# Kernel optimization log

Hardware: AMD Instinct MI355X
Metric: run time of the kernel (lower is better)

Reference implementation:

```python
import jax, jax.numpy as jnp
import numpy as np

EMBED_DIM = 512
Q_DIM = 64
V_DIM = 64
WINDOW_SIZE = 128
B, N = 2, 4096


def setup_inputs() -> dict:
    key = jax.random.key(0)
    ks = jax.random.split(key, 7)
    s = 1.0 / np.sqrt(EMBED_DIM)
    u = lambda k, shape: jax.random.uniform(k, shape, jnp.float32, -s, s)
    return {
        "x": jax.random.normal(ks[0], (B, N, EMBED_DIM), jnp.float32),
        "Wq": u(ks[1], (EMBED_DIM, Q_DIM)),
        "bq": u(ks[2], (Q_DIM,)),
        "Wk": u(ks[3], (EMBED_DIM, Q_DIM)),
        "bk": u(ks[4], (Q_DIM,)),
        "Wv": u(ks[5], (EMBED_DIM, V_DIM)),
        "bv": u(ks[6], (V_DIM,)),
    }


def reference(x, Wq, bq, Wk, bk, Wv, bv):
    b, n, _ = x.shape
    w = WINDOW_SIZE // 2
    Q = x @ Wq + bq  # (b, n, Qd)
    K = x @ Wk + bk  # (b, n, Qd)
    V = x @ Wv + bv  # (b, n, Vd)

    diags = jnp.arange(-w, w + 1)            # (nd,) offsets di
    nd = diags.shape[0]
    # Gather K[i + di] via padded K; invalid positions masked to 0 afterwards.
    Kpad = jnp.pad(K, ((0, 0), (w, w), (0, 0)))
    j = jnp.arange(n)[:, None] + diags[None, :]          # (n, nd) = i + di
    Kg = Kpad[:, j + w, :]                               # (b, n, nd, Qd)
    scores = jnp.einsum('bnd,bnod->bno', Q, Kg)          # (b, n, nd)
    valid = (j >= 0) & (j < n)
    scores = jnp.where(valid[None], scores, 0.0)

    # Faithful to original: diagonal dot products are scattered into the FIRST
    # nd columns of a dense (b, n, n) matrix (rest zeros), softmax over the
    # full n columns, then dense matmul with V.
    columns = jnp.zeros((b, n, n), dtype=x.dtype).at[:, :, :nd].set(scores)
    attn = jax.nn.softmax(columns, axis=2)               # (b, n, n)
    return attn @ V                                      # (b, n, Vd)
```

## Files before the change

kernel.cpp:

```cpp
#include <hip/hip_runtime.h>

typedef _Float16 half8 __attribute__((ext_vector_type(8)));
typedef float f32x4 __attribute__((ext_vector_type(4)));

#define NN 4096
#define NE 512
#define HD 64
#define KROWS 4288
#define KOFF  64
#define WSCALE (1.0f / 256.0f)

__device__ __forceinline__ void f16_split(float f, _Float16& hi, _Float16& lo) {
    hi = (_Float16)f;
    lo = (_Float16)(f - (float)hi);
}

#define MFMA16(a, b, c) __builtin_amdgcn_mfma_f32_16x16x32_f16((a), (b), (c), 0, 0, 0)

__global__ __launch_bounds__(64) void wprep_kernel(
    const float* __restrict__ Wq, const float* __restrict__ Wk,
    const float* __restrict__ Wv,
    _Float16* __restrict__ Wf, _Float16* __restrict__ Khi,
    _Float16* __restrict__ Vf, float* __restrict__ Vs)
{
    const int gtid = blockIdx.x * 64 + threadIdx.x;
    const int L = gtid & 63;
    {
        const int nt = (gtid >> 6) % 12;
        const int kt = gtid / 768;
        const int n = nt * 16 + (L & 15);
        const int kbase = kt * 32 + (L >> 4) * 8;
        const float* src; int col;
        if (n < 64)       { src = Wq; col = n; }
        else if (n < 128) { src = Wk; col = n - 64; }
        else              { src = Wv; col = n - 128; }
        half8 sh;
#pragma unroll
        for (int j = 0; j < 8; ++j)
            sh[j] = (_Float16)src[(size_t)(kbase + j) * HD + col];
        *(half8*)(Wf + (size_t)gtid * 8) = sh;
    }
    if (gtid < 6144) {
        const int p = gtid >> 3, o = gtid & 7;
        const int b = p / 192, q = p - b * 192;
        const size_t row = (size_t)b * KROWS + (q < 64 ? q : 4096 + q);
        const half8 z = {0, 0, 0, 0, 0, 0, 0, 0};
        *(half8*)(Khi + row * HD + o * 8) = z;
    }
    if (gtid < 3200) {
        const int rem = gtid % 1600;
        const int jt = rem / 320;
        const int nt = (rem / 64) % 5;
        half8 sh = {0, 0, 0, 0, 0, 0, 0, 0};
        if (nt == 4 && (L & 15) == 0) {
#pragma unroll
            for (int jj = 0; jj < 8; ++jj) {
                const int j = jt * 32 + (L >> 4) * 8 + jj;
                if (j < 129) sh[jj] = (_Float16)1.0f;
            }
        }
        *(half8*)(Vf + (size_t)gtid * 8) = sh;
    }
    if (gtid < 128) Vs[gtid] = 0.f;
}

__global__ __launch_bounds__(1024, 4) void proj_kernel(
    const float* __restrict__ x, const _Float16* __restrict__ Wf,
    const float* __restrict__ bq, const float* __restrict__ bk,
    const float* __restrict__ bv,
    _Float16* __restrict__ Qhi, _Float16* __restrict__ Qlo,
    _Float16* __restrict__ Khi, _Float16* __restrict__ Vf,
    float* __restrict__ Vs)
{
    __shared__ float parts[2][4][3][64][4];
    __shared__ float V_lds[32][68];
    const int tid = threadIdx.x;
    const int L = tid & 63;
    const int w = tid >> 6;
    const int m = L & 15, kg = L >> 4;
    const int blk = blockIdx.x;
    const int b = blk >> 7;
    const int mt = w >> 3;
    const int t3 = (w >> 1) & 3;
    const int h = w & 1;
    const int r0 = blk * 32;
    const int rr = r0 + mt * 16;

    const float* xp = x + (size_t)(rr + m) * NE + h * 256 + kg * 8;
    const _Float16* wfb = Wf + ((size_t)(h * 8) * 12 + t3 * 3) * 512 + L * 8;

    f32x4 acc[3];
#pragma unroll
    for (int t = 0; t < 3; ++t) acc[t] = (f32x4){0.f, 0.f, 0.f, 0.f};

#pragma unroll
    for (int kt = 0; kt < 8; ++kt) {
        const float4 x0 = *(const float4*)(xp + kt * 32);
        const float4 x1 = *(const float4*)(xp + kt * 32 + 4);
        const float xv[8] = {x0.x, x0.y, x0.z, x0.w, x1.x, x1.y, x1.z, x1.w};
        half8 ahi, alo;
#pragma unroll
        for (int j = 0; j < 8; ++j) {
            _Float16 hh, ll; f16_split(xv[j], hh, ll);
            ahi[j] = hh; alo[j] = ll;
        }
#pragma unroll
        for (int t = 0; t < 3; ++t) {
            const half8 wv = *(const half8*)(wfb + (size_t)kt * 6144 + t * 512);
            acc[t] = MFMA16(ahi, wv, acc[t]);
            acc[t] = MFMA16(alo, wv, acc[t]);
        }
    }

    if (h == 1) {
#pragma unroll
        for (int t = 0; t < 3; ++t)
            *(f32x4*)(&parts[mt][t3][t][L][0]) = acc[t];
    }
    __syncthreads();

    if (h == 0) {
#pragma unroll
        for (int t = 0; t < 3; ++t) {
            const f32x4 p = *(const f32x4*)(&parts[mt][t3][t][L][0]);
            acc[t] += p;
            const int nt = t3 * 3 + t;
            const int cgc = nt * 16 + m;
            const float bias = (cgc < 64) ? bq[cgc]
                             : (cgc < 128) ? bk[cgc - 64] : bv[cgc - 128];
#pragma unroll
            for (int r = 0; r < 4; ++r) {
                const int gr = rr + kg * 4 + r;
                const float val = acc[t][r] + bias;
                if (cgc < 64) {
                    _Float16 hh, ll; f16_split(val, hh, ll);
                    Qhi[(size_t)gr * HD + cgc] = hh;
                    Qlo[(size_t)gr * HD + cgc] = ll;
                } else if (cgc < 128) {
                    const int d = cgc - 64, n = gr & 4095;
                    Khi[((size_t)b * KROWS + KOFF + n) * HD + d] = (_Float16)val;
                } else {
                    V_lds[mt * 16 + kg * 4 + r][cgc - 128] = val;
                }
            }
        }
    }
    __syncthreads();

    if (tid < 64) {
        float s = 0.f;
#pragma unroll
        for (int r = 0; r < 32; ++r) s += V_lds[r][tid];
        atomicAdd(&Vs[b * HD + tid], s);
    }

    {
        const int local = blk & 127;
        if (local < 4 && w < 4) {
            const int jt = local;
            const int nt = w;
            half8 sh;
#pragma unroll
            for (int jj = 0; jj < 8; ++jj)
                sh[jj] = (_Float16)V_lds[kg * 8 + jj][nt * 16 + m];
            const size_t fo = ((size_t)((b * 25 + jt * 5 + nt) * 64 + L)) * 8;
            *(half8*)(Vf + fo) = sh;
        } else if (local == 4 && w < 4 && kg == 0) {
            const int nt = w;
            half8 sh = {0, 0, 0, 0, 0, 0, 0, 0};
            sh[0] = (_Float16)V_lds[0][nt * 16 + m];
            const size_t fo = ((size_t)((b * 25 + 4 * 5 + nt) * 64 + L)) * 8;
            *(half8*)(Vf + fo) = sh;
        }
    }
}

__global__ __launch_bounds__(512) void attn_kernel(
    const _Float16* __restrict__ Qhi, const _Float16* __restrict__ Qlo,
    const _Float16* __restrict__ Khi, const _Float16* __restrict__ Vf,
    const float* __restrict__ Vs, float* __restrict__ out)
{
    __shared__ __align__(16) _Float16 wt_hi[32 * 168];
    __shared__ __align__(16) _Float16 wt_lo[32 * 168];
    __shared__ float den_lds[32];

    const int tid = threadIdx.x;
    const int L = tid & 63;
    const int w = tid >> 6;
    const int m = L & 15, kg = L >> 4;
    const int b = blockIdx.x >> 7;
    const int n0 = (blockIdx.x & 127) * 32;
    const int qt = w & 1;
    const int mt = w >> 2;
    const int nt = w & 3;
    const bool den_wave = (w == 0) || (w == 6);

    const float vs = Vs[b * HD + nt * 16 + m];

    const _Float16* qp  = Qhi + ((size_t)(b * NN + n0 + qt * 16 + m)) * HD + kg * 8;
    const _Float16* qp2 = Qlo + ((size_t)(b * NN + n0 + qt * 16 + m)) * HD + kg * 8;
    const half8 qhi0 = *(const half8*)(qp);
    const half8 qhi1 = *(const half8*)(qp + 32);
    const half8 qlo0 = *(const half8*)(qp2);
    const half8 qlo1 = *(const half8*)(qp2 + 32);

    const int i4 = w >> 1;
    const int f = (i4 == 0) ? 1 : (i4 == 1) ? 2 : (i4 == 2) ? 0 : 3;
    int kts[3]; int nkt;
    kts[0] = f + qt; kts[1] = f + qt + 4; kts[2] = f + qt + 8;
    nkt = (i4 == 2) ? 3 : 2;

    const _Float16* KB = Khi + (size_t)b * KROWS * HD;
    half8 kh0[3], kh1[3];
#pragma unroll
    for (int i = 0; i < 3; ++i) {
        if (i < nkt) {
            const _Float16* kp = KB + (size_t)(n0 + kts[i] * 16 + m) * HD + kg * 8;
            kh0[i] = *(const half8*)(kp);
            kh1[i] = *(const half8*)(kp + 32);
        }
    }

    half8 vhi[5], vh4[5];
#pragma unroll
    for (int jt = 0; jt < 5; ++jt) {
        const size_t fo = ((size_t)((b * 25 + jt * 5 + nt) * 64 + L)) * 8;
        vhi[jt] = *(const half8*)(Vf + fo);
    }
    if (den_wave) {
#pragma unroll
        for (int jt = 0; jt < 5; ++jt) {
            const size_t fo4 = ((size_t)((b * 25 + jt * 5 + 4) * 64 + L)) * 8;
            vh4[jt] = *(const half8*)(Vf + fo4);
        }
    }

    for (int t = tid; t < 2048; t += 512) {
        const int bufsel = t >= 1024;
        const int idx = t & 1023;
        const int q = idx >> 5;
        const int j = 129 + (idx & 31);
        (bufsel ? wt_lo : wt_hi)[q * 168 + j] = (_Float16)0.f;
    }

#pragma unroll
    for (int i = 0; i < 3; ++i) {
        if (i < nkt) {
            f32x4 acc = (f32x4){0.f, 0.f, 0.f, 0.f};
            acc = MFMA16(qhi0, kh0[i], acc);
            acc = MFMA16(qhi1, kh1[i], acc);
            acc = MFMA16(qlo0, kh0[i], acc);
            acc = MFMA16(qlo1, kh1[i], acc);
            const int l = kts[i] * 16 + m;
#pragma unroll
            for (int r = 0; r < 4; ++r) {
                const int q = qt * 16 + kg * 4 + r;
                const int j = l - q;
                if (j >= 0 && j < 129) {
                    const float wval = (__expf(acc[r]) - 1.0f) * WSCALE;
                    _Float16 hh, ll; f16_split(wval, hh, ll);
                    wt_hi[q * 168 + j] = hh;
                    wt_lo[q * 168 + j] = ll;
                }
            }
        }
    }
    __syncthreads();

    f32x4 oacc = (f32x4){0.f, 0.f, 0.f, 0.f};
    f32x4 dacc = (f32x4){0.f, 0.f, 0.f, 0.f};
#pragma unroll
    for (int jt = 0; jt < 5; ++jt) {
        const half8 whi = *(const half8*)(wt_hi + (mt * 16 + m) * 168 + jt * 32 + kg * 8);
        const half8 wlo = *(const half8*)(wt_lo + (mt * 16 + m) * 168 + jt * 32 + kg * 8);
        oacc = MFMA16(whi, vhi[jt], oacc);
        oacc = MFMA16(wlo, vhi[jt], oacc);
        if (den_wave) {
            dacc = MFMA16(whi, vh4[jt], dacc);
            dacc = MFMA16(wlo, vh4[jt], dacc);
        }
    }
    if (den_wave && m == 0) {
#pragma unroll
        for (int r = 0; r < 4; ++r) den_lds[mt * 16 + kg * 4 + r] = dacc[r];
    }
    __syncthreads();

    {
#pragma unroll
        for (int r = 0; r < 4; ++r) {
            const int q = mt * 16 + kg * 4 + r;
            const float val = (vs + 256.0f * oacc[r])
                            / (4096.f + 256.0f * den_lds[q]);
            out[((size_t)(b * NN + n0 + q)) * HD + nt * 16 + m] = val;
        }
    }
}

extern "C" void kernel_launch(void* const* d_in, const int* in_sizes, int n_in,
                              void* d_out, int out_size, void* d_ws, size_t ws_size,
                              hipStream_t stream)
{
    const float* x  = (const float*)d_in[0];
    const float* Wq = (const float*)d_in[1];
    const float* bq = (const float*)d_in[2];
    const float* Wk = (const float*)d_in[3];
    const float* bk = (const float*)d_in[4];
    const float* Wv = (const float*)d_in[5];
    const float* bv = (const float*)d_in[6];
    float* out = (float*)d_out;

    char* ws = (char*)d_ws;
    float*     Vs  = (float*)(ws + 0);
    _Float16*  Khi = (_Float16*)(ws + 512);
    _Float16*  Qhi = (_Float16*)(ws + 1098240);
    _Float16*  Qlo = (_Float16*)(ws + 2146816);
    _Float16*  Wf  = (_Float16*)(ws + 3195392);
    _Float16*  Vf  = (_Float16*)(ws + 3392000);

    wprep_kernel<<<192, 64, 0, stream>>>(Wq, Wk, Wv, Wf, Khi, Vf, Vs);
    proj_kernel<<<256, 1024, 0, stream>>>(x, Wf, bq, bk, bv,
                                          Qhi, Qlo, Khi, Vf, Vs);
    attn_kernel<<<256, 512, 0, stream>>>(Qhi, Qlo, Khi, Vf, Vs, out);
}
```

Measured before the change: 94.76 us.

## Reuse projection weights across two row tiles and drop denominator LDS barrier

The projection kernel now has each wave handle both 16-row tiles over a quarter of the embedding dimension. Each loaded weight fragment therefore feeds twice as many MFMAs, and the partial sums are reduced across four K-splits through a larger LDS buffer. In the attention kernel every wave computes the softmax denominator itself and broadcasts it with a wavefront shuffle, which removes the den_lds array and a __syncthreads. The cost is redundant denominator MFMAs and extra vh4 loads in all waves, plus more accumulator registers and LDS in the projection kernel.

```diff
diff --git a/kernel.cpp b/kernel.cpp
--- a/kernel.cpp
+++ b/kernel.cpp
@@ -72,7 +72,7 @@
     _Float16* __restrict__ Khi, _Float16* __restrict__ Vf,
     float* __restrict__ Vs)
 {
-    __shared__ float parts[2][4][3][64][4];
+    __shared__ float parts[3][4][2][3][64][4];
     __shared__ float V_lds[32][68];
     const int tid = threadIdx.x;
     const int L = tid & 63;
@@ -80,58 +80,70 @@
     const int m = L & 15, kg = L >> 4;
     const int blk = blockIdx.x;
     const int b = blk >> 7;
-    const int mt = w >> 3;
-    const int t3 = (w >> 1) & 3;
-    const int h = w & 1;
+    const int t3 = w & 3;
+    const int h4 = w >> 2;
     const int r0 = blk * 32;
-    const int rr = r0 + mt * 16;
-
-    const float* xp = x + (size_t)(rr + m) * NE + h * 256 + kg * 8;
-    const _Float16* wfb = Wf + ((size_t)(h * 8) * 12 + t3 * 3) * 512 + L * 8;
-
-    f32x4 acc[3];
-#pragma unroll
-    for (int t = 0; t < 3; ++t) acc[t] = (f32x4){0.f, 0.f, 0.f, 0.f};
-
-#pragma unroll
-    for (int kt = 0; kt < 8; ++kt) {
-        const float4 x0 = *(const float4*)(xp + kt * 32);
-        const float4 x1 = *(const float4*)(xp + kt * 32 + 4);
-        const float xv[8] = {x0.x, x0.y, x0.z, x0.w, x1.x, x1.y, x1.z, x1.w};
-        half8 ahi, alo;
+
+    const float* xp = x + (size_t)(r0 + m) * NE + h4 * 128 + kg * 8;
+    const _Float16* wfb = Wf + ((size_t)(h4 * 4) * 12 + t3 * 3) * 512 + L * 8;
+
+    f32x4 acc[2][3];
+#pragma unroll
+    for (int rt = 0; rt < 2; ++rt)
+#pragma unroll
+        for (int t = 0; t < 3; ++t) acc[rt][t] = (f32x4){0.f, 0.f, 0.f, 0.f};
+
+#pragma unroll
+    for (int kt = 0; kt < 4; ++kt) {
+        const float4 a0 = *(const float4*)(xp + kt * 32);
+        const float4 a1 = *(const float4*)(xp + kt * 32 + 4);
+        const float4 c0 = *(const float4*)(xp + 16 * NE + kt * 32);
+        const float4 c1 = *(const float4*)(xp + 16 * NE + kt * 32 + 4);
+        const float av[8] = {a0.x, a0.y, a0.z, a0.w, a1.x, a1.y, a1.z, a1.w};
+        const float cv[8] = {c0.x, c0.y, c0.z, c0.w, c1.x, c1.y, c1.z, c1.w};
+        half8 ahi, alo, chi, clo;
 #pragma unroll
         for (int j = 0; j < 8; ++j) {
-            _Float16 hh, ll; f16_split(xv[j], hh, ll);
-            ahi[j] = hh; alo[j] = ll;
+            _Float16 hh, ll;
+            f16_split(av[j], hh, ll); ahi[j] = hh; alo[j] = ll;
+            f16_split(cv[j], hh, ll); chi[j] = hh; clo[j] = ll;
         }
 #pragma unroll
         for (int t = 0; t < 3; ++t) {
             const half8 wv = *(const half8*)(wfb + (size_t)kt * 6144 + t * 512);
-            acc[t] = MFMA16(ahi, wv, acc[t]);
-            acc[t] = MFMA16(alo, wv, acc[t]);
-        }
-    }
-
-    if (h == 1) {
-#pragma unroll
-        for (int t = 0; t < 3; ++t)
-            *(f32x4*)(&parts[mt][t3][t][L][0]) = acc[t];
+            acc[0][t] = MFMA16(ahi, wv, acc[0][t]);
+            acc[0][t] = MFMA16(alo, wv, acc[0][t]);
+            acc[1][t] = MFMA16(chi, wv, acc[1][t]);
+            acc[1][t] = MFMA16(clo, wv, acc[1][t]);
+        }
+    }
+
+    if (h4 != 0) {
+#pragma unroll
+        for (int rt = 0; rt < 2; ++rt)
+#pragma unroll
+            for (int t = 0; t < 3; ++t)
+                *(f32x4*)(&parts[h4 - 1][t3][rt][t][L][0]) = acc[rt][t];
     }
     __syncthreads();
 
-    if (h == 0) {
+    if (h4 == 0) {
+#pragma unroll
+        for (int rt = 0; rt < 2; ++rt)
 #pragma unroll
         for (int t = 0; t < 3; ++t) {
-            const f32x4 p = *(const f32x4*)(&parts[mt][t3][t][L][0]);
-            acc[t] += p;
+            f32x4 s = acc[rt][t];
+#pragma unroll
+            for (int p = 0; p < 3; ++p)
+                s += *(const f32x4*)(&parts[p][t3][rt][t][L][0]);
             const int nt = t3 * 3 + t;
             const int cgc = nt * 16 + m;
             const float bias = (cgc < 64) ? bq[cgc]
                              : (cgc < 128) ? bk[cgc - 64] : bv[cgc - 128];
 #pragma unroll
             for (int r = 0; r < 4; ++r) {
-                const int gr = rr + kg * 4 + r;
-                const float val = acc[t][r] + bias;
+                const int gr = r0 + rt * 16 + kg * 4 + r;
+                const float val = s[r] + bias;
                 if (cgc < 64) {
                     _Float16 hh, ll; f16_split(val, hh, ll);
                     Qhi[(size_t)gr * HD + cgc] = hh;
@@ -140,7 +152,7 @@
                     const int d = cgc - 64, n = gr & 4095;
                     Khi[((size_t)b * KROWS + KOFF + n) * HD + d] = (_Float16)val;
                 } else {
-                    V_lds[mt * 16 + kg * 4 + r][cgc - 128] = val;
+                    V_lds[rt * 16 + kg * 4 + r][cgc - 128] = val;
                 }
             }
         }
@@ -182,7 +194,6 @@
 {
     __shared__ __align__(16) _Float16 wt_hi[32 * 168];
     __shared__ __align__(16) _Float16 wt_lo[32 * 168];
-    __shared__ float den_lds[32];
 
     const int tid = threadIdx.x;
     const int L = tid & 63;
@@ -193,7 +204,6 @@
     const int qt = w & 1;
     const int mt = w >> 2;
     const int nt = w & 3;
-    const bool den_wave = (w == 0) || (w == 6);
 
     const float vs = Vs[b * HD + nt * 16 + m];
 
@@ -226,13 +236,8 @@
     for (int jt = 0; jt < 5; ++jt) {
         const size_t fo = ((size_t)((b * 25 + jt * 5 + nt) * 64 + L)) * 8;
         vhi[jt] = *(const half8*)(Vf + fo);
-    }
-    if (den_wave) {
-#pragma unroll
-        for (int jt = 0; jt < 5; ++jt) {
-            const size_t fo4 = ((size_t)((b * 25 + jt * 5 + 4) * 64 + L)) * 8;
-            vh4[jt] = *(const half8*)(Vf + fo4);
-        }
+        const size_t fo4 = ((size_t)((b * 25 + jt * 5 + 4) * 64 + L)) * 8;
+        vh4[jt] = *(const half8*)(Vf + fo4);
     }
 
     for (int t = tid; t < 2048; t += 512) {
@@ -275,23 +280,21 @@
         const half8 wlo = *(const half8*)(wt_lo + (mt * 16 + m) * 168 + jt * 32 + kg * 8);
         oacc = MFMA16(whi, vhi[jt], oacc);
         oacc = MFMA16(wlo, vhi[jt], oacc);
-        if (den_wave) {
-            dacc = MFMA16(whi, vh4[jt], dacc);
-            dacc = MFMA16(wlo, vh4[jt], dacc);
-        }
-    }
-    if (den_wave && m == 0) {
-#pragma unroll
-        for (int r = 0; r < 4; ++r) den_lds[mt * 16 + kg * 4 + r] = dacc[r];
-    }
-    __syncthreads();
+        dacc = MFMA16(whi, vh4[jt], dacc);
+        dacc = MFMA16(wlo, vh4[jt], dacc);
+    }
+
+    float den[4];
+#pragma unroll
+    for (int r = 0; r < 4; ++r)
+        den[r] = __shfl(dacc[r], L & 48, 64);
 
     {
 #pragma unroll
         for (int r = 0; r < 4; ++r) {
             const int q = mt * 16 + kg * 4 + r;
             const float val = (vs + 256.0f * oacc[r])
-                            / (4096.f + 256.0f * den_lds[q]);
+                            / (4096.f + 256.0f * den[r]);
             out[((size_t)(b * NN + n0 + q)) * HD + nt * 16 + m] = val;
         }
     }
```

New measurement: 94.50 us. About the same (-0.3%).
